# Performance work log

Measured on AMD Instinct MI355X. Metric: run time of the kernel, lower is better.

## Reference

```python
import jax, jax.numpy as jnp
import numpy as np

NUM_LAYER = 3
NUM_GRAPHS = 512
EMB = 128
EDGE_DIM = 16
BN_EPS = 1e-5


def setup_inputs() -> dict:
    key = jax.random.key(0)
    ks = jax.random.split(key, 24)
    N, E = 100000, 600000
    s = 0.02
    inp = {
        'input_feature': jax.random.normal(ks[0], (N, EMB), jnp.float32),
        'edge_attr': jax.random.normal(ks[1], (E, EDGE_DIM), jnp.float32),
        'edge_index': jax.random.randint(ks[2], (2, E), 0, N, jnp.int64),
        'batch': jnp.sort(jax.random.randint(ks[3], (N,), 0, NUM_GRAPHS, jnp.int64)),
        # virtual node embedding, initialized to zero as in the torch module
        'vn_emb': jnp.zeros((1, EMB), jnp.float32),
        # GIN conv params per layer (edge encoder + 2-layer MLP)
        'conv_edge_w': s * jax.random.normal(ks[4], (NUM_LAYER, EDGE_DIM, EMB), jnp.float32),
        'conv_edge_b': jnp.zeros((NUM_LAYER, EMB), jnp.float32),
        'conv_w1': s * jax.random.normal(ks[5], (NUM_LAYER, EMB, 2 * EMB), jnp.float32),
        'conv_b1': jnp.zeros((NUM_LAYER, 2 * EMB), jnp.float32),
        'conv_w2': s * jax.random.normal(ks[6], (NUM_LAYER, 2 * EMB, EMB), jnp.float32),
        'conv_b2': jnp.zeros((NUM_LAYER, EMB), jnp.float32),
        # outer BatchNorm affine params (eval mode: running_mean=0, running_var=1)
        'bn_gamma': 1.0 + s * jax.random.normal(ks[7], (NUM_LAYER, EMB), jnp.float32),
        'bn_beta': s * jax.random.normal(ks[8], (NUM_LAYER, EMB), jnp.float32),
        # virtual-node MLP params (num_layer-1 of them)
        'vn_w1': s * jax.random.normal(ks[9], (NUM_LAYER - 1, EMB, 2 * EMB), jnp.float32),
        'vn_b1': jnp.zeros((NUM_LAYER - 1, 2 * EMB), jnp.float32),
        'vn_g1': jnp.ones((NUM_LAYER - 1, 2 * EMB), jnp.float32),
        'vn_be1': jnp.zeros((NUM_LAYER - 1, 2 * EMB), jnp.float32),
        'vn_w2': s * jax.random.normal(ks[10], (NUM_LAYER - 1, 2 * EMB, EMB), jnp.float32),
        'vn_b2': jnp.zeros((NUM_LAYER - 1, EMB), jnp.float32),
        'vn_g2': jnp.ones((NUM_LAYER - 1, EMB), jnp.float32),
        'vn_be2': jnp.zeros((NUM_LAYER - 1, EMB), jnp.float32),
    }
    return inp


def _forward(input_feature, edge_attr, vn_emb, conv_edge_w, conv_edge_b,
             conv_w1, conv_b1, conv_w2, conv_b2, bn_gamma, bn_beta,
             vn_w1, vn_b1, vn_g1, vn_be1, vn_w2, vn_b2, vn_g2, vn_be2,
             edge_index, batch):
    N = input_feature.shape[0]
    src, dst = edge_index[0], edge_index[1]
    inv = 1.0 / jnp.sqrt(jnp.asarray(1.0 + BN_EPS, input_feature.dtype))  # eval BN: mean 0, var 1
    vn = jnp.broadcast_to(vn_emb, (NUM_GRAPHS, EMB))  # one shared learned row
    h = input_feature
    for l in range(NUM_LAYER):
        h_in = h + vn[batch]  # gather virtual node per graph
        # GIN conv: msg = relu(x_src + edge_embedding), scatter-add to dst
        edge_emb = edge_attr @ conv_edge_w[l] + conv_edge_b[l]  # [E, D]
        msg = jax.nn.relu(h_in[src] + edge_emb)
        agg = jax.ops.segment_sum(msg, dst, num_segments=N)
        z = h_in + agg  # (1 + eps) * x + agg with eps = 0
        z = jax.nn.relu(z @ conv_w1[l] + conv_b1[l]) @ conv_w2[l] + conv_b2[l]
        z = z * (bn_gamma[l] * inv) + bn_beta[l]  # eval BatchNorm
        if l < NUM_LAYER - 1:
            z = jax.nn.relu(z)
        z = z + h_in  # residual (dropout is identity in eval mode)
        if l < NUM_LAYER - 1:
            vt = jax.ops.segment_sum(h_in, batch, num_segments=NUM_GRAPHS) + vn
            m = jax.nn.relu((vt @ vn_w1[l] + vn_b1[l]) * (vn_g1[l] * inv) + vn_be1[l])
            m = jax.nn.relu((m @ vn_w2[l] + vn_b2[l]) * (vn_g2[l] * inv) + vn_be2[l])
            vn = vn + m  # residual=True path
        h = z
    return h  # JK == 'last'


def reference(input_feature, edge_index, edge_attr, batch, vn_emb, conv_edge_w,
              conv_edge_b, conv_w1, conv_b1, conv_w2, conv_b2, bn_gamma, bn_beta,
              vn_w1, vn_b1, vn_g1, vn_be1, vn_w2, vn_b2, vn_g2, vn_be2):
    return _forward(input_feature, edge_attr, vn_emb, conv_edge_w, conv_edge_b,
                    conv_w1, conv_b1, conv_w2, conv_b2, bn_gamma, bn_beta,
                    vn_w1, vn_b1, vn_g1, vn_be1, vn_w2, vn_b2, vn_g2, vn_be2,
                    edge_index, batch)
```

## Files before the change

kernel.cpp:

```cpp
#include <hip/hip_runtime.h>
#include <math.h>
#include <stdint.h>

#define EMB 128
#define HID 256
#define ED 16
#define NGRAPH 512
#define NLAYER 3
#define VT_CHUNK 64
#define NPW 8

typedef unsigned short ushort_t;
typedef __attribute__((ext_vector_type(8))) short short8;
typedef __attribute__((ext_vector_type(4))) float fx4;
typedef __attribute__((ext_vector_type(4))) unsigned int uint4v;

__device__ __forceinline__ ushort_t f2b(float f){
  unsigned int u = __builtin_bit_cast(unsigned int, f);
  unsigned int r = u + 0x7FFFu + ((u >> 16) & 1u);
  return (ushort_t)(r >> 16);
}
__device__ __forceinline__ float b2f(ushort_t u){
  return __builtin_bit_cast(float, ((unsigned int)u) << 16);
}
__device__ __forceinline__ float blo(unsigned int u){
  return __builtin_bit_cast(float, u << 16);
}
__device__ __forceinline__ float bhi(unsigned int u){
  return __builtin_bit_cast(float, u & 0xFFFF0000u);
}

__device__ __forceinline__ float dot2b(unsigned int a, unsigned int b, float c){
  float r = c;
  asm("v_dot2_f32_bf16 %0, %1, %2, %0" : "+v"(r) : "v"(a), "v"(b));
  return r;
}

__device__ __forceinline__ float2 dot16(uint4v u0, uint4v u1,
                                        const unsigned int* wp0, const unsigned int* wp1,
                                        float be0, float be1){
  unsigned int uu[8] = {u0[0], u0[1], u0[2], u0[3], u1[0], u1[1], u1[2], u1[3]};
  float e0 = be0, e1 = be1;
  #pragma unroll
  for (int k = 0; k < 8; k++){
    e0 = dot2b(uu[k], wp0[k], e0);
    e1 = dot2b(uu[k], wp1[k], e1);
  }
  return make_float2(e0, e1);
}

__global__ void k_init_vn(float* __restrict__ vn, const float* __restrict__ vn_emb){
  int idx = blockIdx.x * 256 + threadIdx.x;
  vn[idx] = vn_emb[idx & (EMB - 1)];
}

__global__ void k_transw(const float* __restrict__ w1, const float* __restrict__ w2,
                         ushort_t* __restrict__ w1t, ushort_t* __restrict__ w2t){
  int idx = blockIdx.x * 256 + threadIdx.x;
  if (idx >= NLAYER * EMB * HID) return;
  int l = idx / (EMB * HID);
  int r = idx % (EMB * HID);
  { int k = r / HID, n = r % HID; w1t[(l * HID + n) * EMB + k] = f2b(w1[idx]); }
  { int k = r / EMB, n = r % EMB; w2t[(l * EMB + n) * HID + k] = f2b(w2[idx]); }
}

__global__ void k_count(const int* __restrict__ dst, int* __restrict__ counts,
                        int* __restrict__ rankv, int E){
  int e = blockIdx.x * 256 + threadIdx.x;
  if (e >= E) return;
  rankv[e] = atomicAdd(&counts[dst[e]], 1);
}

__global__ void k_scanA(const int* __restrict__ counts, int* __restrict__ offs,
                        int* __restrict__ bsum, int N){
  __shared__ int sdata[256];
  int t = threadIdx.x;
  int base = blockIdx.x * 2048 + t * 8;
  int v[8]; int s = 0;
  #pragma unroll
  for (int j = 0; j < 8; j++){
    int idx = base + j;
    v[j] = (idx < N) ? counts[idx] : 0;
    s += v[j];
  }
  sdata[t] = s; __syncthreads();
  for (int off = 1; off < 256; off <<= 1){
    int x = (t >= off) ? sdata[t - off] : 0;
    __syncthreads();
    sdata[t] += x;
    __syncthreads();
  }
  int incl = sdata[t];
  int run = incl - s;
  #pragma unroll
  for (int j = 0; j < 8; j++){
    int idx = base + j;
    if (idx < N) offs[idx] = run;
    run += v[j];
  }
  if (t == 255) bsum[blockIdx.x] = incl;
}

__global__ void k_scanB(const int* __restrict__ bsum, int* __restrict__ boff, int nb){
  __shared__ int sdata[256];
  int t = threadIdx.x;
  int v = (t < nb) ? bsum[t] : 0;
  sdata[t] = v; __syncthreads();
  for (int off = 1; off < 256; off <<= 1){
    int x = (t >= off) ? sdata[t - off] : 0;
    __syncthreads();
    sdata[t] += x;
    __syncthreads();
  }
  if (t < nb) boff[t] = sdata[t] - v;
}

__global__ void k_scanC(int* __restrict__ offs, const int* __restrict__ boff, int N, int E){
  int i = blockIdx.x * 256 + threadIdx.x;
  if (i < N) offs[i] += boff[i >> 11];
  else if (i == N) offs[N] = E;
}

__global__ void k_reorder(const float* __restrict__ ea, const int* __restrict__ src,
                          const int* __restrict__ dst, const int* __restrict__ rankv,
                          const int* __restrict__ offs, ushort_t* __restrict__ ea2,
                          int* __restrict__ srcs, int E){
  int e = blockIdx.x * 256 + threadIdx.x;
  if (e >= E) return;
  int pos = offs[dst[e]] + rankv[e];
  srcs[pos] = src[e];
  const float4* p = (const float4*)(ea + (size_t)e * ED);
  float4 f0 = p[0], f1 = p[1], f2 = p[2], f3 = p[3];
  float f[ED] = {f0.x, f0.y, f0.z, f0.w, f1.x, f1.y, f1.z, f1.w,
                 f2.x, f2.y, f2.z, f2.w, f3.x, f3.y, f3.z, f3.w};
  unsigned int u[8];
  #pragma unroll
  for (int k = 0; k < 8; k++)
    u[k] = (unsigned int)f2b(f[2 * k]) | ((unsigned int)f2b(f[2 * k + 1]) << 16);
  uint4* q = (uint4*)(ea2 + (size_t)pos * ED);
  q[0] = make_uint4(u[0], u[1], u[2], u[3]);
  q[1] = make_uint4(u[4], u[5], u[6], u[7]);
}

__global__ void k_hin(const float* __restrict__ h, const int* __restrict__ batch,
                      const float* __restrict__ vn, ushort_t* __restrict__ hb, int N){
  int idx = blockIdx.x * 256 + threadIdx.x;
  if (idx >= N * 32) return;
  int node = idx >> 5;
  int c = (idx & 31) * 4;
  float4 hv = *(const float4*)(h + (size_t)node * EMB + c);
  int b = batch[node];
  float4 v = *(const float4*)(vn + b * EMB + c);
  uint2 ob;
  ob.x = (unsigned int)f2b(hv.x + v.x) | ((unsigned int)f2b(hv.y + v.y) << 16);
  ob.y = (unsigned int)f2b(hv.z + v.z) | ((unsigned int)f2b(hv.w + v.w) << 16);
  *(uint2*)(hb + (size_t)node * EMB + c) = ob;
}

__global__ __launch_bounds__(256) void k_agg(const ushort_t* __restrict__ hb,
                      const ushort_t* __restrict__ ea2,
                      const int* __restrict__ srcs, const int* __restrict__ offs,
                      const float* __restrict__ We, const float* __restrict__ be,
                      ushort_t* __restrict__ z0, float* __restrict__ vt,
                      int zerovt, int N){
  if (zerovt){
    int idx = blockIdx.x * 256 + threadIdx.x;
    if (idx < NGRAPH * EMB) vt[idx] = 0.f;
  }
  int lane = threadIdx.x & 63;
  int wid = (blockIdx.x * blockDim.x + threadIdx.x) >> 6;
  int n0 = wid * NPW;
  if (n0 >= N) return;
  int nn = N - n0; if (nn > NPW) nn = NPW;
  int c0 = lane * 2;

  unsigned int wp0[8], wp1[8];
  #pragma unroll
  for (int k = 0; k < 8; k++){
    wp0[k] = (unsigned int)f2b(We[(2 * k) * EMB + c0])
           | ((unsigned int)f2b(We[(2 * k + 1) * EMB + c0]) << 16);
    wp1[k] = (unsigned int)f2b(We[(2 * k) * EMB + c0 + 1])
           | ((unsigned int)f2b(We[(2 * k + 1) * EMB + c0 + 1]) << 16);
  }
  float be0 = be[c0], be1 = be[c0 + 1];

  int j    = offs[n0];
  int cend = offs[n0 + 1];
  int jend = offs[n0 + nn];
  int ni = 0;
  unsigned int hn = *(const unsigned int*)(hb + (size_t)n0 * EMB + c0);
  float ax = 0.f, ay = 0.f;

  auto flush = [&](){
    while (j == cend && ni < nn){
      float r0 = blo(hn) + ax, r1 = bhi(hn) + ay;
      unsigned int outv = (unsigned int)f2b(r0) | ((unsigned int)f2b(r1) << 16);
      *(unsigned int*)(z0 + (size_t)(n0 + ni) * EMB + c0) = outv;
      ni++;
      if (ni < nn){
        hn = *(const unsigned int*)(hb + (size_t)(n0 + ni) * EMB + c0);
        cend = offs[n0 + ni + 1];
        ax = 0.f; ay = 0.f;
      }
    }
  };

  auto do1 = [&](unsigned int g){
    const uint4v* p = (const uint4v*)(ea2 + (size_t)j * ED);
    uint4v u0 = p[0], u1 = p[1];
    float2 m = dot16(u0, u1, wp0, wp1, be0, be1);
    ax += fmaxf(blo(g) + m.x, 0.f);
    ay += fmaxf(bhi(g) + m.y, 0.f);
    j++; flush();
  };

  auto do4 = [&](unsigned int gA, unsigned int gB, unsigned int gC, unsigned int gD){
    const uint4v* p = (const uint4v*)(ea2 + (size_t)j * ED);
    uint4v uA0 = p[0], uA1 = p[1];
    uint4v uB0 = p[2], uB1 = p[3];
    uint4v uC0 = p[4], uC1 = p[5];
    uint4v uD0 = p[6], uD1 = p[7];
    float2 mA = dot16(uA0, uA1, wp0, wp1, be0, be1);
    float2 mB = dot16(uB0, uB1, wp0, wp1, be0, be1);
    float2 mC = dot16(uC0, uC1, wp0, wp1, be0, be1);
    float2 mD = dot16(uD0, uD1, wp0, wp1, be0, be1);
    ax += fmaxf(blo(gA) + mA.x, 0.f);  ay += fmaxf(bhi(gA) + mA.y, 0.f);  j++; flush();
    ax += fmaxf(blo(gB) + mB.x, 0.f);  ay += fmaxf(bhi(gB) + mB.y, 0.f);  j++; flush();
    ax += fmaxf(blo(gC) + mC.x, 0.f);  ay += fmaxf(bhi(gC) + mC.y, 0.f);  j++; flush();
    ax += fmaxf(blo(gD) + mD.x, 0.f);  ay += fmaxf(bhi(gD) + mD.y, 0.f);  j++; flush();
  };

  flush();

  if (j + 8 <= jend){
    int sA = srcs[j],     sB = srcs[j + 1], sC = srcs[j + 2], sD = srcs[j + 3];
    int nA = srcs[j + 4], nB = srcs[j + 5], nC = srcs[j + 6], nD = srcs[j + 7];
    unsigned int gA = *(const unsigned int*)(hb + (size_t)sA * EMB + c0);
    unsigned int gB = *(const unsigned int*)(hb + (size_t)sB * EMB + c0);
    unsigned int gC = *(const unsigned int*)(hb + (size_t)sC * EMB + c0);
    unsigned int gD = *(const unsigned int*)(hb + (size_t)sD * EMB + c0);

    while (j + 12 <= jend){
      const uint4v* p = (const uint4v*)(ea2 + (size_t)j * ED);
      uint4v uA0 = p[0], uA1 = p[1];
      uint4v uB0 = p[2], uB1 = p[3];
      uint4v uC0 = p[4], uC1 = p[5];
      uint4v uD0 = p[6], uD1 = p[7];
      unsigned int hA = *(const unsigned int*)(hb + (size_t)nA * EMB + c0);
      unsigned int hB = *(const unsigned int*)(hb + (size_t)nB * EMB + c0);
      unsigned int hC = *(const unsigned int*)(hb + (size_t)nC * EMB + c0);
      unsigned int hD = *(const unsigned int*)(hb + (size_t)nD * EMB + c0);
      int tA = srcs[j + 8], tB = srcs[j + 9], tC = srcs[j + 10], tD = srcs[j + 11];
      float2 mA = dot16(uA0, uA1, wp0, wp1, be0, be1);
      float2 mB = dot16(uB0, uB1, wp0, wp1, be0, be1);
      float2 mC = dot16(uC0, uC1, wp0, wp1, be0, be1);
      float2 mD = dot16(uD0, uD1, wp0, wp1, be0, be1);
      ax += fmaxf(blo(gA) + mA.x, 0.f);  ay += fmaxf(bhi(gA) + mA.y, 0.f);  j++; flush();
      ax += fmaxf(blo(gB) + mB.x, 0.f);  ay += fmaxf(bhi(gB) + mB.y, 0.f);  j++; flush();
      ax += fmaxf(blo(gC) + mC.x, 0.f);  ay += fmaxf(bhi(gC) + mC.y, 0.f);  j++; flush();
      ax += fmaxf(blo(gD) + mD.x, 0.f);  ay += fmaxf(bhi(gD) + mD.y, 0.f);  j++; flush();
      gA = hA; gB = hB; gC = hC; gD = hD;
      nA = tA; nB = tB; nC = tC; nD = tD;
    }
    do4(gA, gB, gC, gD);
    gA = *(const unsigned int*)(hb + (size_t)nA * EMB + c0);
    gB = *(const unsigned int*)(hb + (size_t)nB * EMB + c0);
    gC = *(const unsigned int*)(hb + (size_t)nC * EMB + c0);
    gD = *(const unsigned int*)(hb + (size_t)nD * EMB + c0);
    do4(gA, gB, gC, gD);
  }
  while (j < jend){
    int s = srcs[j];
    unsigned int g = *(const unsigned int*)(hb + (size_t)s * EMB + c0);
    do1(g);
  }
}

__global__ __launch_bounds__(256, 2) void k_mlp(const ushort_t* __restrict__ A,
                                                const ushort_t* __restrict__ w1t,
                                                const float* __restrict__ b1,
                                                const ushort_t* __restrict__ w2t,
                                                const float* __restrict__ b2,
                                                const float* __restrict__ gamma,
                                                const float* __restrict__ beta,
                                                const ushort_t* __restrict__ hb_in,
                                                const int* __restrict__ batch,
                                                const float* __restrict__ vn_next,
                                                ushort_t* __restrict__ hb_out,
                                                float* __restrict__ fout,
                                                float inv, int last, int ntiles, int N){
  __shared__ ushort_t ts[2][16][264];
  int w = threadIdx.x >> 6, lane = threadIdx.x & 63;
  int m = lane & 15, q = lane >> 4;

  short8 w1f[4][4];
  #pragma unroll
  for (int kk = 0; kk < 4; kk++)
    #pragma unroll
    for (int t = 0; t < 4; t++)
      w1f[kk][t] = *(const short8*)(w1t + (size_t)(w * 64 + t * 16 + m) * EMB + kk * 32 + q * 8);
  short8 w2f[8][2];
  #pragma unroll
  for (int kk = 0; kk < 8; kk++)
    #pragma unroll
    for (int t = 0; t < 2; t++)
      w2f[kk][t] = *(const short8*)(w2t + (size_t)(w * 32 + t * 16 + m) * HID + kk * 32 + q * 8);

  float bv1[4], bv2[2], sc2[2], bt2[2];
  #pragma unroll
  for (int t = 0; t < 4; t++) bv1[t] = b1[w * 64 + t * 16 + m];
  #pragma unroll
  for (int t = 0; t < 2; t++){
    int c = w * 32 + t * 16 + m;
    bv2[t] = b2[c]; sc2[t] = gamma[c] * inv; bt2[t] = beta[c];
  }

  int tile = blockIdx.x;
  if (tile >= ntiles) return;
  short8 a_cur[4];
  #pragma unroll
  for (int kk = 0; kk < 4; kk++)
    a_cur[kk] = *(const short8*)(A + (size_t)(tile * 16 + m) * EMB + kk * 32 + q * 8);

  int p = 0;
  for (; tile < ntiles; tile += gridDim.x, p ^= 1){
    int row_base = tile * 16;
    fx4 acc[4];
    #pragma unroll
    for (int t = 0; t < 4; t++) acc[t] = fx4{0.f, 0.f, 0.f, 0.f};
    #pragma unroll
    for (int kk = 0; kk < 4; kk++){
      #pragma unroll
      for (int t = 0; t < 4; t++)
        acc[t] = __builtin_amdgcn_mfma_f32_16x16x32_bf16(a_cur[kk], w1f[kk][t], acc[t], 0, 0, 0);
    }
    {
      int nt = tile + gridDim.x;
      int nb = (nt < ntiles) ? nt * 16 : 0;
      #pragma unroll
      for (int kk = 0; kk < 4; kk++)
        a_cur[kk] = *(const short8*)(A + (size_t)(nb + m) * EMB + kk * 32 + q * 8);
    }
    int b_r[4]; ushort_t h_r[4][2];
    #pragma unroll
    for (int i = 0; i < 4; i++){
      int r = row_base + q * 4 + i;
      if (r >= N) r = N - 1;
      b_r[i] = last ? 0 : batch[r];
      #pragma unroll
      for (int t = 0; t < 2; t++)
        h_r[i][t] = hb_in[(size_t)r * EMB + w * 32 + t * 16 + m];
    }
    #pragma unroll
    for (int t = 0; t < 4; t++){
      int c = w * 64 + t * 16 + m;
      #pragma unroll
      for (int i = 0; i < 4; i++)
        ts[p][q * 4 + i][c] = f2b(fmaxf(acc[t][i] + bv1[t], 0.f));
    }
    __syncthreads();
    float vnv[4][2];
    if (!last){
      #pragma unroll
      for (int i = 0; i < 4; i++)
        #pragma unroll
        for (int t = 0; t < 2; t++)
          vnv[i][t] = vn_next[b_r[i] * EMB + w * 32 + t * 16 + m];
    }
    fx4 acc2[2];
    #pragma unroll
    for (int t = 0; t < 2; t++) acc2[t] = fx4{0.f, 0.f, 0.f, 0.f};
    #pragma unroll
    for (int kk = 0; kk < 8; kk++){
      short8 a = *(const short8*)(&ts[p][m][kk * 32 + q * 8]);
      #pragma unroll
      for (int t = 0; t < 2; t++)
        acc2[t] = __builtin_amdgcn_mfma_f32_16x16x32_bf16(a, w2f[kk][t], acc2[t], 0, 0, 0);
    }
    #pragma unroll
    for (int i = 0; i < 4; i++){
      int r = row_base + q * 4 + i;
      if (r >= N) continue;
      #pragma unroll
      for (int t = 0; t < 2; t++){
        int c = w * 32 + t * 16 + m;
        float v = acc2[t][i] + bv2[t];
        v = v * sc2[t] + bt2[t];
        if (!last) v = fmaxf(v, 0.f);
        v += b2f(h_r[i][t]);
        if (!last){
          v += vnv[i][t];
          hb_out[(size_t)r * EMB + c] = f2b(v);
        } else {
          fout[(size_t)r * EMB + c] = v;
        }
      }
    }
  }
}

__global__ void k_vt(const ushort_t* __restrict__ hb, const int* __restrict__ batch,
                     float* __restrict__ vt, int N){
  int c = threadIdx.x & 127;
  int half = threadIdx.x >> 7;
  int start = blockIdx.x * VT_CHUNK;
  int end = start + VT_CHUNK; if (end > N) end = N;
  float acc = 0.f;
  int curg = batch[start];
  for (int i = start + half; i < end; i += 2){
    int g = batch[i];
    if (g != curg){
      atomicAdd(&vt[curg * EMB + c], acc);
      acc = 0.f;
      curg = g;
    }
    acc += b2f(hb[(size_t)i * EMB + c]);
  }
  atomicAdd(&vt[curg * EMB + c], acc);
}

__global__ void k_vnmlp(const float* __restrict__ vt,
                        const float* __restrict__ w1, const float* __restrict__ b1,
                        const float* __restrict__ g1, const float* __restrict__ be1,
                        const float* __restrict__ w2, const float* __restrict__ b2,
                        const float* __restrict__ g2, const float* __restrict__ be2,
                        const float* __restrict__ vnc, float* __restrict__ vnn, float inv){
  __shared__ float vs[EMB];
  __shared__ float ms[HID];
  int g = blockIdx.x, t = threadIdx.x;
  if (t < EMB) vs[t] = vt[g * EMB + t] + vnc[g * EMB + t];
  __syncthreads();
  float acc = b1[t];
  #pragma unroll 4
  for (int k = 0; k < EMB; k++) acc = fmaf(vs[k], w1[k * HID + t], acc);
  acc = acc * (g1[t] * inv) + be1[t];
  ms[t] = fmaxf(acc, 0.f);
  __syncthreads();
  if (t < EMB){
    float a2 = b2[t];
    #pragma unroll 4
    for (int k = 0; k < HID; k++) a2 = fmaf(ms[k], w2[k * EMB + t], a2);
    a2 = a2 * (g2[t] * inv) + be2[t];
    vnn[g * EMB + t] = vnc[g * EMB + t] + fmaxf(a2, 0.f);
  }
}

extern "C" void kernel_launch(void* const* d_in, const int* in_sizes, int n_in,
                              void* d_out, int out_size, void* d_ws, size_t ws_size,
                              hipStream_t stream){
  const float* in_feat   = (const float*)d_in[0];
  const float* edge_attr = (const float*)d_in[1];
  const int*   eidx      = (const int*)d_in[2];
  const int*   batch     = (const int*)d_in[3];
  const float* vn_emb    = (const float*)d_in[4];
  const float* cew = (const float*)d_in[5];
  const float* ceb = (const float*)d_in[6];
  const float* cw1 = (const float*)d_in[7];
  const float* cb1 = (const float*)d_in[8];
  const float* cw2 = (const float*)d_in[9];
  const float* cb2 = (const float*)d_in[10];
  const float* bng = (const float*)d_in[11];
  const float* bnb = (const float*)d_in[12];
  const float* vw1 = (const float*)d_in[13];
  const float* vb1 = (const float*)d_in[14];
  const float* vg1 = (const float*)d_in[15];
  const float* vbe1 = (const float*)d_in[16];
  const float* vw2 = (const float*)d_in[17];
  const float* vb2 = (const float*)d_in[18];
  const float* vg2 = (const float*)d_in[19];
  const float* vbe2 = (const float*)d_in[20];
  float* out = (float*)d_out;

  int N = in_sizes[0] / EMB;
  int E = in_sizes[2] / 2;
  const int* src = eidx;
  const int* dst = eidx + E;

  char* ws = (char*)d_ws;
  auto alloc = [&](size_t bytes) -> char* {
    char* p = ws; ws += (bytes + 255) & ~(size_t)255; return p;
  };
  ushort_t* z0    = (ushort_t*)alloc((size_t)N * EMB * 2);
  ushort_t* hb    = (ushort_t*)alloc((size_t)N * EMB * 2);
  ushort_t* ea2   = (ushort_t*)alloc((size_t)E * ED * 2);
  int*      srcs  = (int*)alloc((size_t)E * 4);
  float*    vn0   = (float*)alloc((size_t)NGRAPH * EMB * 4);
  float*    vn1   = (float*)alloc((size_t)NGRAPH * EMB * 4);
  float*    vt    = (float*)alloc((size_t)NGRAPH * EMB * 4);
  int*      counts = (int*)alloc((size_t)N * 4);
  int*      rankv  = (int*)alloc((size_t)E * 4);
  int*      offs   = (int*)alloc(((size_t)N + 1) * 4);
  int*      bsum   = (int*)alloc(256 * 4);
  int*      boff   = (int*)alloc(256 * 4);
  ushort_t* w1t = (ushort_t*)alloc((size_t)NLAYER * HID * EMB * 2);
  ushort_t* w2t = (ushort_t*)alloc((size_t)NLAYER * EMB * HID * 2);
  float* vnbuf[2] = {vn0, vn1};

  float inv = 1.0f / sqrtf(1.0f + 1e-5f);
  int ntiles = (N + 15) / 16;
  int nagg = (N + NPW * 4 - 1) / (NPW * 4);

  hipMemsetAsync(counts, 0, (size_t)N * 4, stream);
  k_init_vn<<<NGRAPH * EMB / 256, 256, 0, stream>>>(vn0, vn_emb);
  k_transw<<<(NLAYER * EMB * HID + 255) / 256, 256, 0, stream>>>(cw1, cw2, w1t, w2t);
  k_count<<<(E + 255) / 256, 256, 0, stream>>>(dst, counts, rankv, E);
  int nsb = (N + 2047) / 2048;
  k_scanA<<<nsb, 256, 0, stream>>>(counts, offs, bsum, N);
  k_scanB<<<1, 256, 0, stream>>>(bsum, boff, nsb);
  k_scanC<<<(N + 1 + 255) / 256, 256, 0, stream>>>(offs, boff, N, E);
  k_reorder<<<(E + 255) / 256, 256, 0, stream>>>(edge_attr, src, dst, rankv, offs, ea2, srcs, E);

  for (int l = 0; l < NLAYER; l++){
    const float* vnc = vnbuf[l & 1];
    float* vnn = vnbuf[(l + 1) & 1];
    int last = (l == NLAYER - 1) ? 1 : 0;
    if (l == 0)
      k_hin<<<(N * 32 + 255) / 256, 256, 0, stream>>>(in_feat, batch, vnc, hb, N);
    k_agg<<<nagg, 256, 0, stream>>>(hb, ea2, srcs, offs,
                                    cew + (size_t)l * ED * EMB, ceb + (size_t)l * EMB,
                                    z0, vt, !last, N);
    if (!last){
      k_vt<<<(N + VT_CHUNK - 1) / VT_CHUNK, 256, 0, stream>>>(hb, batch, vt, N);
      k_vnmlp<<<NGRAPH, HID, 0, stream>>>(vt,
                                          vw1 + (size_t)l * EMB * HID, vb1 + (size_t)l * HID,
                                          vg1 + (size_t)l * HID, vbe1 + (size_t)l * HID,
                                          vw2 + (size_t)l * HID * EMB, vb2 + (size_t)l * EMB,
                                          vg2 + (size_t)l * EMB, vbe2 + (size_t)l * EMB,
                                          vnc, vnn, inv);
    }
    k_mlp<<<1024, 256, 0, stream>>>(z0, w1t + (size_t)l * HID * EMB, cb1 + (size_t)l * HID,
                                    w2t + (size_t)l * EMB * HID, cb2 + (size_t)l * EMB,
                                    bng + (size_t)l * EMB, bnb + (size_t)l * EMB,
                                    hb, batch, vnn, hb, out, inv, last, ntiles, N);
  }
}
```

Before: 719.5 us.

## Fuse virtual-node segment sum into aggregation kernel via per-node atomics

Removes the separate k_vt kernel and instead accumulates each node's hidden vector into the per-graph vt buffer from inside k_agg, when the node's output row is written. The vt zeroing moves from inside k_agg to a hipMemsetAsync before it. This saves one kernel launch and a full re-read of hb. In exchange it issues two float atomics per node per lane with no local pre-reduction, about 100k×128 atomics spread over only 512 graphs, so contention on vt addresses may be high.

```diff
diff --git a/kernel.cpp b/kernel.cpp
--- a/kernel.cpp
+++ b/kernel.cpp
@@ -7,7 +7,6 @@
 #define ED 16
 #define NGRAPH 512
 #define NLAYER 3
-#define VT_CHUNK 64
 #define NPW 8
 
 typedef unsigned short ushort_t;
@@ -162,11 +161,7 @@
                       const int* __restrict__ srcs, const int* __restrict__ offs,
                       const float* __restrict__ We, const float* __restrict__ be,
                       ushort_t* __restrict__ z0, float* __restrict__ vt,
-                      int zerovt, int N){
-  if (zerovt){
-    int idx = blockIdx.x * 256 + threadIdx.x;
-    if (idx < NGRAPH * EMB) vt[idx] = 0.f;
-  }
+                      const int* __restrict__ batch, int dovt, int N){
   int lane = threadIdx.x & 63;
   int wid = (blockIdx.x * blockDim.x + threadIdx.x) >> 6;
   int n0 = wid * NPW;
@@ -196,6 +191,11 @@
       float r0 = blo(hn) + ax, r1 = bhi(hn) + ay;
       unsigned int outv = (unsigned int)f2b(r0) | ((unsigned int)f2b(r1) << 16);
       *(unsigned int*)(z0 + (size_t)(n0 + ni) * EMB + c0) = outv;
+      if (dovt){
+        int b = batch[n0 + ni];
+        atomicAdd(&vt[b * EMB + c0], blo(hn));
+        atomicAdd(&vt[b * EMB + c0 + 1], bhi(hn));
+      }
       ni++;
       if (ni < nn){
         hn = *(const unsigned int*)(hb + (size_t)(n0 + ni) * EMB + c0);
@@ -397,26 +397,6 @@
       }
     }
   }
-}
-
-__global__ void k_vt(const ushort_t* __restrict__ hb, const int* __restrict__ batch,
-                     float* __restrict__ vt, int N){
-  int c = threadIdx.x & 127;
-  int half = threadIdx.x >> 7;
-  int start = blockIdx.x * VT_CHUNK;
-  int end = start + VT_CHUNK; if (end > N) end = N;
-  float acc = 0.f;
-  int curg = batch[start];
-  for (int i = start + half; i < end; i += 2){
-    int g = batch[i];
-    if (g != curg){
-      atomicAdd(&vt[curg * EMB + c], acc);
-      acc = 0.f;
-      curg = g;
-    }
-    acc += b2f(hb[(size_t)i * EMB + c]);
-  }
-  atomicAdd(&vt[curg * EMB + c], acc);
 }
 
 __global__ void k_vnmlp(const float* __restrict__ vt,
@@ -516,11 +496,12 @@
     int last = (l == NLAYER - 1) ? 1 : 0;
     if (l == 0)
       k_hin<<<(N * 32 + 255) / 256, 256, 0, stream>>>(in_feat, batch, vnc, hb, N);
+    if (!last)
+      hipMemsetAsync(vt, 0, (size_t)NGRAPH * EMB * 4, stream);
     k_agg<<<nagg, 256, 0, stream>>>(hb, ea2, srcs, offs,
                                     cew + (size_t)l * ED * EMB, ceb + (size_t)l * EMB,
-                                    z0, vt, !last, N);
+                                    z0, vt, batch, !last, N);
     if (!last){
-      k_vt<<<(N + VT_CHUNK - 1) / VT_CHUNK, 256, 0, stream>>>(hb, batch, vt, N);
       k_vnmlp<<<NGRAPH, HID, 0, stream>>>(vt,
                                           vw1 + (size_t)l * EMB * HID, vb1 + (size_t)l * HID,
                                           vg1 + (size_t)l * HID, vbe1 + (size_t)l * HID,
```

New measurement: 790.6 us. 9.9% more time.
